# Optimization experiments

Measured on AMD Instinct MI355X. Metric: run time of the kernel, lower is better.

The kernel has to match this reference:

```python
import jax, jax.numpy as jnp
import numpy as np

RADIUS = 2.0      # ball radius (meters)
NSAMPLE = 32      # max neighbors per ball
B = 4             # number of scenes (batch)
NPB = 4096        # points per scene (equal counts assumed)
C = 20            # number of semantic classes
CUBE = 20.0       # points live in a [0,20]^3 m cube


def setup_inputs() -> dict:
    key = jax.random.key(0)
    k1, k2, k3 = jax.random.split(key, 3)
    xyz = jax.random.uniform(k1, (B * NPB, 3), jnp.float32) * CUBE
    pred = jax.random.normal(k2, (B * NPB, C), jnp.float32)
    labels = jax.random.randint(k3, (B * NPB,), 0, C)
    tgt = jax.nn.one_hot(labels, C, dtype=jnp.float32)
    cnt = jnp.full((B,), NPB, dtype=jnp.int32)
    # module asserts new_xyz == xyz and equal batch counts
    return {"xyz": xyz, "xyz_batch_cnt": cnt, "pred": pred, "tgt": tgt,
            "new_xyz": xyz, "new_xyz_batch_cnt": cnt}


def _ball_query(xyz_b, new_xyz_b, radius, nsample):
    """xyz_b, new_xyz_b: (B, n, 3). Returns local idx (B, n, nsample).
    Replicates pointnet2 stack ball_query: first `nsample` points (in index
    order) with squared distance < radius^2; unfilled slots repeat the first
    found index. Indices are local to each batch segment."""
    n = xyz_b.shape[1]
    d2 = jnp.sum((new_xyz_b[:, :, None, :] - xyz_b[:, None, :, :]) ** 2, axis=-1)  # (B,n,n)
    mask = d2 < radius * radius
    # score = point index if inside ball else sentinel n; smallest scores = first hits
    score = jnp.where(mask, jnp.arange(n, dtype=jnp.int32), jnp.int32(n))
    neg_vals, _ = jax.lax.top_k(-score, nsample)   # largest of -score == smallest score
    idx = -neg_vals                                # (B,n,nsample), ascending index order
    first = idx[:, :, :1]                          # first found index (self is always in-ball)
    idx = jnp.where(idx == n, first, idx)          # fill empty slots with first index
    return idx


def _group(feats_b, idx_b):
    """feats_b: (B, n, C); idx_b: (B, m, nsample) local indices -> (B, m, nsample, C)."""
    b = jnp.arange(feats_b.shape[0])[:, None, None]
    return feats_b[b, idx_b]


def reference(xyz, xyz_batch_cnt, pred, tgt, new_xyz, new_xyz_batch_cnt):
    nb = xyz_batch_cnt.shape[0]
    n = xyz.shape[0] // nb                 # equal per-batch counts
    xyz_b = xyz.reshape(nb, n, 3)
    new_xyz_b = new_xyz.reshape(nb, n, 3)

    idx_b = _ball_query(xyz_b, new_xyz_b, RADIUS, NSAMPLE)   # (B,n,ns)
    m = nb * n
    idx = idx_b.reshape(m, NSAMPLE)

    # grouping_operation -> (M, C, nsample)
    grouped_pred = _group(pred.reshape(nb, n, -1), idx_b).reshape(m, NSAMPLE, -1).transpose(0, 2, 1)
    grouped_tgt = _group(tgt.reshape(nb, n, -1), idx_b).reshape(m, NSAMPLE, -1).transpose(0, 2, 1)

    # since new_xyz == xyz, every ball contains its own center -> empty_ball_mask
    # is all-False and the nonempty filtering in the torch code is the identity.
    pred_local_relation = grouped_pred - pred[:, :, None]
    tgt_local_relation = grouped_tgt - tgt[:, :, None]

    # weight (computed under no_grad in torch)
    eq = idx == idx[:, :1]
    not_eq = ~eq
    not_eq = not_eq.at[:, 0].set(True)
    a = not_eq.astype(jnp.float32)
    weight = a / jnp.sum(a, axis=-1, keepdims=True)
    return (pred_local_relation, tgt_local_relation, weight)
```

## Files before the change

kernel.cpp:

```cpp
#include <hip/hip_runtime.h>

#define NS 32
#define GD 10
#define NCXY (GD * GD)
#define COLCAP 128
#define WCAP 64
#define INV_CELL 0.5f
#define MARGIN 1e-3f

static __device__ __forceinline__ int lane_rank(unsigned long long m) {
    return __builtin_amdgcn_mbcnt_hi((unsigned)(m >> 32),
                                     __builtin_amdgcn_mbcnt_lo((unsigned)m, 0u));
}

__global__ __launch_bounds__(256) void build_kernel(
    const float* __restrict__ xyz, int n,
    int* __restrict__ colOff, float4* __restrict__ pts)
{
    __shared__ float4 hl[4][WCAP];
    __shared__ int    swcnt[4];
    __shared__ float4 merged[COLCAP];

    const int col  = blockIdx.x;
    const int b    = col / NCXY;
    const int cxy  = col - b * NCXY;
    const int mycx = cxy / GD;
    const int mycy = cxy - mycx * GD;
    const int lane = threadIdx.x & 63;
    const int wv   = threadIdx.x >> 6;
    const float* __restrict__ px = xyz + (size_t)b * n * 3;

    const int per = (n + 3) >> 2;
    const int j0  = wv * per;
    const int j1  = min(j0 + per, n);
    int cnt = 0;
    for (int it = j0; it < j1; it += 64) {
        const int  j   = it + lane;
        const bool inb = j < j1;
        const int  jc  = inb ? j : 0;
        const float x = px[3 * jc], y = px[3 * jc + 1], z = px[3 * jc + 2];
        const int cx = min(max((int)floorf(x * INV_CELL), 0), GD - 1);
        const int cy = min(max((int)floorf(y * INV_CELL), 0), GD - 1);
        const bool hit = inb && (cx == mycx) && (cy == mycy);
        const unsigned long long m = __ballot(hit);
        if (m) {
            const int zc  = min(max((int)floorf(z * INV_CELL), 0), GD - 1);
            const int pos = cnt + lane_rank(m);
            if (hit && pos < WCAP)
                hl[wv][pos] = make_float4(x, y, z, __int_as_float((zc << 12) | j));
            cnt += __popcll(m);
        }
    }
    if (lane == 0) swcnt[wv] = cnt < WCAP ? cnt : WCAP;
    __syncthreads();

    const int p0 = swcnt[0], p1 = p0 + swcnt[1], p2 = p1 + swcnt[2], p3 = p2 + swcnt[3];
    const int h  = p3 < COLCAP ? p3 : COLCAP;
    if (wv == 0) {
        for (int g = lane; g < h; g += 64) {
            const int w   = (g >= p0) + (g >= p1) + (g >= p2);
            const int off = g - (w == 0 ? 0 : (w == 1 ? p0 : (w == 2 ? p1 : p2)));
            merged[g] = hl[w][off];
        }
    }
    __syncthreads();

    if (wv == 0) {
        int czc[GD];
        #pragma unroll
        for (int k = 0; k < GD; ++k) czc[k] = 0;
        for (int r = 0; r < h; r += 64) {
            const int t = r + lane;
            int zc = -1;
            if (t < h) zc = __float_as_int(merged[t].w) >> 12;
            #pragma unroll
            for (int k = 0; k < GD; ++k)
                czc[k] += __popcll(__ballot(zc == k));
        }
        int off[GD + 1];
        off[0] = 0;
        #pragma unroll
        for (int k = 0; k < GD; ++k) off[k + 1] = off[k] + czc[k];

        int cur[GD];
        #pragma unroll
        for (int k = 0; k < GD; ++k) cur[k] = off[k];

        for (int r = 0; r < h; r += 64) {
            const int t = r + lane;
            int zc = -1, pl = 0;
            float4 f = make_float4(0.f, 0.f, 0.f, 0.f);
            if (t < h) { f = merged[t]; pl = __float_as_int(f.w); zc = pl >> 12; }
            #pragma unroll
            for (int k = 0; k < GD; ++k) {
                const unsigned long long mk = __ballot(zc == k);
                if (zc == k) {
                    const int pos = cur[k] + lane_rank(mk);
                    pts[(size_t)col * COLCAP + pos] =
                        make_float4(f.x, f.y, f.z, __int_as_float(pl & 4095));
                }
                cur[k] += __popcll(mk);
            }
        }
        if (lane == 0) {
            const int bo = col * 11;
            #pragma unroll
            for (int k = 0; k < GD; ++k) colOff[bo + k] = off[k];
            colOff[bo + GD] = h;
        }
    }
}

template <int C>
__global__ __launch_bounds__(256) void query_kernel(
    const float* __restrict__ new_xyz,
    const float* __restrict__ pred, const float* __restrict__ tgt,
    const int* __restrict__ colOff, const float4* __restrict__ pts,
    int n, int total,
    float* __restrict__ out0, float* __restrict__ out1, float* __restrict__ wout)
{
#pragma clang fp contract(off)
    __shared__ int spref[4][17];
    __shared__ int sgb[4][16];
    __shared__ int slist[4][64];

    const int lane = threadIdx.x & 63;
    const int wv   = __builtin_amdgcn_readfirstlane(threadIdx.x >> 6);
    int q = blockIdx.x * 4 + wv;
    if (q >= total) q = total - 1;
    const int b    = q / n;
    const int base = b * n;

    const float qx = new_xyz[q * 3 + 0];
    const float qy = new_xyz[q * 3 + 1];
    const float qz = new_xyz[q * 3 + 2];

    int cx0 = max((int)floorf((qx - 2.0f - MARGIN) * INV_CELL), 0);
    int cx1 = min((int)floorf((qx + 2.0f + MARGIN) * INV_CELL), GD - 1);
    int cy0 = max((int)floorf((qy - 2.0f - MARGIN) * INV_CELL), 0);
    int cy1 = min((int)floorf((qy + 2.0f + MARGIN) * INV_CELL), GD - 1);
    int cz0 = max((int)floorf((qz - 2.0f - MARGIN) * INV_CELL), 0);
    int cz1 = min((int)floorf((qz + 2.0f + MARGIN) * INV_CELL), GD - 1);
    const int ny = cy1 - cy0 + 1;
    const int nrange = __builtin_amdgcn_readfirstlane((cx1 - cx0 + 1) * ny);

    int cc = 0, gb = 0;
    if (lane < nrange) {
        const int rx   = lane / ny;
        const int ry   = lane - rx * ny;
        const int ccol = b * NCXY + (cx0 + rx) * GD + (cy0 + ry);
        const int o0   = colOff[ccol * 11 + cz0];
        const int o1   = colOff[ccol * 11 + cz1 + 1];
        gb = ccol * COLCAP + o0;
        cc = o1 - o0;
    }
    int run = cc;
    #pragma unroll
    for (int off = 1; off < 64; off <<= 1) {
        int y = __shfl_up(run, off, 64);
        if (lane >= off) run += y;
    }
    const int T = __shfl(run, nrange - 1, 64);

    if (lane < 16) spref[wv][lane + 1] = run;
    if (lane == 0) spref[wv][0] = 0;
    if (lane < nrange) sgb[wv][lane] = gb;

    __syncthreads();

    int tot = 0;
    for (int r = 0; r < T; r += 64) {
        const int  t   = r + lane;
        const bool act = t < T;
        const int  tcl = act ? t : 0;
        int k = 0;
        #pragma unroll
        for (int step = 8; step >= 1; step >>= 1) {
            const int nk = k + step;
            if (spref[wv][nk] <= tcl) k = nk;
        }
        const int ai = sgb[wv][k] + (tcl - spref[wv][k]);
        const float4 f = pts[ai];
        float dx = qx - f.x, dy = qy - f.y, dz = qz - f.z;
        float d2 = (dx * dx + dy * dy) + dz * dz;
        const bool hit = act && (d2 < 4.0f);
        const unsigned long long m = __ballot(hit);
        const int pos = tot + lane_rank(m);
        if (hit && pos < 64) slist[wv][pos] = __float_as_int(f.w);
        tot += __popcll(m);
    }

    __syncthreads();

    const int totv = tot < 64 ? tot : 64;
    int v = (lane < totv) ? slist[wv][lane] : 0x7fffffff;
    const int l32 = lane & 31;
    if (totv <= 32) {
        #pragma unroll
        for (int k = 2; k <= 32; k <<= 1) {
            #pragma unroll
            for (int j = k >> 1; j >= 1; j >>= 1) {
                const int  o     = __shfl_xor(v, j, 32);
                const bool up    = ((l32 & k) == 0);
                const bool lower = ((l32 & j) == 0);
                const int  mn = v < o ? v : o;
                const int  mx = v < o ? o : v;
                v = (lower == up) ? mn : mx;
            }
        }
    } else {
        #pragma unroll
        for (int k = 2; k <= 64; k <<= 1) {
            #pragma unroll
            for (int j = k >> 1; j >= 1; j >>= 1) {
                const int  o     = __shfl_xor(v, j, 64);
                const bool up    = ((lane & k) == 0);
                const bool lower = ((lane & j) == 0);
                const int  mn = v < o ? v : o;
                const int  mx = v < o ? o : v;
                v = (lower == up) ? mn : mx;
            }
        }
    }

    const int tc     = tot < NS ? tot : NS;
    const int firstv = __shfl(v, 0, 64);
    const int first  = (tot > 0) ? firstv : (n - 1);
    const int s      = lane & 31;
    const int jl0    = __shfl(v, s, 64);
    const int jl     = (s < tc) ? jl0 : first;

    const int tcm = tc > 0 ? tc : 1;
    if (lane < NS)
        wout[(size_t)q * NS + lane] = (lane < tcm) ? 1.0f / (float)tcm : 0.0f;

    const float* __restrict__ src = (lane >> 5) ? tgt : pred;
    float* __restrict__ dst       = (lane >> 5) ? out1 : out0;
    const float4* __restrict__ nb = (const float4*)(src + (size_t)(base + jl) * C);
    const float4* __restrict__ ct = (const float4*)(src + (size_t)q * C);
    float* __restrict__ o = dst + (size_t)q * (C * NS) + s;
    #pragma unroll
    for (int c4 = 0; c4 < C / 4; ++c4) {
        const float4 a = nb[c4], bq = ct[c4];
        o[(c4 * 4 + 0) * NS] = a.x - bq.x;
        o[(c4 * 4 + 1) * NS] = a.y - bq.y;
        o[(c4 * 4 + 2) * NS] = a.z - bq.z;
        o[(c4 * 4 + 3) * NS] = a.w - bq.w;
    }
    #pragma unroll
    for (int c = (C / 4) * 4; c < C; ++c)
        o[c * NS] = src[(size_t)(base + jl) * C + c] - src[(size_t)q * C + c];
}

template <int C>
__global__ __launch_bounds__(256) void fused_brute_kernel(
    const float* __restrict__ xyz, const float* __restrict__ new_xyz,
    const float* __restrict__ pred, const float* __restrict__ tgt,
    int n, int total, float* __restrict__ out0, float* __restrict__ out1,
    float* __restrict__ wout)
{
#pragma clang fp contract(off)
    __shared__ int sidx[8][NS];

    const int lane = threadIdx.x & 63;
    const int wv   = __builtin_amdgcn_readfirstlane(threadIdx.x >> 6);
    int q0 = (blockIdx.x * 4 + wv) * 2;
    if (q0 > total - 2) q0 = total - 2;
    const int base = (q0 / n) * n;

    const float ax0 = new_xyz[q0 * 3 + 0], ay0 = new_xyz[q0 * 3 + 1], az0 = new_xyz[q0 * 3 + 2];
    const float ax1 = new_xyz[q0 * 3 + 3], ay1 = new_xyz[q0 * 3 + 4], az1 = new_xyz[q0 * 3 + 5];
    const float* __restrict__ px = xyz + (size_t)base * 3;

    int tot0 = 0, tot1 = 0, first0 = n - 1, first1 = n - 1;
    for (int it = 0; it < n; it += 64) {
        const int ja  = it + lane;
        const int jca = ja < n ? ja : n - 1;
        const float xa = px[jca * 3 + 0], ya = px[jca * 3 + 1], za = px[jca * 3 + 2];
        float dx = ax0 - xa, dy = ay0 - ya, dz = az0 - za;
        const float d0 = (dx * dx + dy * dy) + dz * dz;
        dx = ax1 - xa; dy = ay1 - ya; dz = az1 - za;
        const float d1 = (dx * dx + dy * dy) + dz * dz;
        const bool h0 = (ja < n) & (d0 < 4.0f);
        const bool h1 = (ja < n) & (d1 < 4.0f);
        const unsigned long long m0 = __ballot(h0);
        if (m0) {
            if (tot0 == 0) first0 = it + __builtin_ctzll(m0);
            const int pos = tot0 + lane_rank(m0);
            if (h0 && pos < NS) sidx[wv * 2 + 0][pos] = ja;
            tot0 += __popcll(m0);
        }
        const unsigned long long m1 = __ballot(h1);
        if (m1) {
            if (tot1 == 0) first1 = it + __builtin_ctzll(m1);
            const int pos = tot1 + lane_rank(m1);
            if (h1 && pos < NS) sidx[wv * 2 + 1][pos] = ja;
            tot1 += __popcll(m1);
        }
    }

    const int s  = lane & 31;
    const int qs = lane >> 5;
    {
        const int tt    = qs ? tot1 : tot0;
        const int first = qs ? first1 : first0;
        const int tc    = tt < NS ? tt : NS;
        if (s >= tc) sidx[wv * 2 + qs][s] = first;
        const int tcm = tc > 0 ? tc : 1;
        wout[(size_t)q0 * NS + lane] = (s < tcm) ? 1.0f / (float)tcm : 0.0f;
    }
    __syncthreads();

    const int q  = q0 + qs;
    const int jl = sidx[wv * 2 + qs][s];
    const float4* __restrict__ nb_p = (const float4*)(pred + (size_t)(base + jl) * C);
    const float4* __restrict__ nb_t = (const float4*)(tgt  + (size_t)(base + jl) * C);
    const float4* __restrict__ ct_p = (const float4*)(pred + (size_t)q * C);
    const float4* __restrict__ ct_t = (const float4*)(tgt  + (size_t)q * C);
    float* __restrict__ o0 = out0 + (size_t)q * (C * NS) + s;
    float* __restrict__ o1 = out1 + (size_t)q * (C * NS) + s;
    #pragma unroll
    for (int c4 = 0; c4 < C / 4; ++c4) {
        const float4 a = nb_p[c4], bq = ct_p[c4];
        o0[(c4 * 4 + 0) * NS] = a.x - bq.x;
        o0[(c4 * 4 + 1) * NS] = a.y - bq.y;
        o0[(c4 * 4 + 2) * NS] = a.z - bq.z;
        o0[(c4 * 4 + 3) * NS] = a.w - bq.w;
        const float4 u = nb_t[c4], vv = ct_t[c4];
        o1[(c4 * 4 + 0) * NS] = u.x - vv.x;
        o1[(c4 * 4 + 1) * NS] = u.y - vv.y;
        o1[(c4 * 4 + 2) * NS] = u.z - vv.z;
        o1[(c4 * 4 + 3) * NS] = u.w - vv.w;
    }
}

extern "C" void kernel_launch(void* const* d_in, const int* in_sizes, int n_in,
                              void* d_out, int out_size, void* d_ws, size_t ws_size,
                              hipStream_t stream)
{
    const float* xyz     = (const float*)d_in[0];
    const float* pred    = (const float*)d_in[2];
    const float* tgt     = (const float*)d_in[3];
    const float* new_xyz = (const float*)d_in[4];

    const int total = in_sizes[0] / 3;
    const int nb    = in_sizes[1];
    const int n     = total / nb;
    const int C     = in_sizes[2] / total;

    float* out = (float*)d_out;
    const size_t relsz = (size_t)total * C * NS;
    float* out0 = out;
    float* out1 = out + relsz;
    float* wout = out + 2 * relsz;

    const int ncols = nb * NCXY;
    const size_t ws_need = (size_t)ncols * COLCAP * sizeof(float4)
                         + (size_t)ncols * 11 * sizeof(int);

    if (C == 20 && ws_size >= ws_need) {
        float4* pts    = (float4*)d_ws;
        int*    colOff = (int*)((char*)d_ws + (size_t)ncols * COLCAP * sizeof(float4));

        build_kernel<<<ncols, 256, 0, stream>>>(xyz, n, colOff, pts);
        query_kernel<20><<<(total + 3) / 4, 256, 0, stream>>>(
            new_xyz, pred, tgt, colOff, pts, n, total, out0, out1, wout);
    } else if (C == 20) {
        fused_brute_kernel<20><<<(total + 7) / 8, 256, 0, stream>>>(
            xyz, new_xyz, pred, tgt, n, total, out0, out1, wout);
    }
    (void)n_in; (void)out_size;
}
```

Before: 37.17 us.

## Process two query points per wavefront in grid ball-query kernel

The query kernel now handles two queries per 64-lane wave. Cell ranges for both are scanned in half-waves, and candidate loads and distance tests for the two queries are interleaved in one loop. The neighbour lists are sorted with 32-lane bitonic sorts in parallel, then staged through shared memory so all 64 lanes write weights and gathered outputs for both queries. This aims to raise lane utilisation and memory-level parallelism, at the cost of more registers, an extra barrier, and a fallback to the brute-force kernel when n is not a multiple of 8.

```diff
diff --git a/kernel.cpp b/kernel.cpp
--- a/kernel.cpp
+++ b/kernel.cpp
@@ -112,7 +112,7 @@
 }
 
 template <int C>
-__global__ __launch_bounds__(256) void query_kernel(
+__global__ __launch_bounds__(256) void query2_kernel(
     const float* __restrict__ new_xyz,
     const float* __restrict__ pred, const float* __restrict__ tgt,
     const int* __restrict__ colOff, const float4* __restrict__ pts,
@@ -120,136 +120,188 @@
     float* __restrict__ out0, float* __restrict__ out1, float* __restrict__ wout)
 {
 #pragma clang fp contract(off)
-    __shared__ int spref[4][17];
-    __shared__ int sgb[4][16];
-    __shared__ int slist[4][64];
+    __shared__ int spref[4][2][17];
+    __shared__ int sgb[4][2][16];
+    __shared__ int slist[4][2][64];
+    __shared__ int sorted[4][2][32];
 
     const int lane = threadIdx.x & 63;
     const int wv   = __builtin_amdgcn_readfirstlane(threadIdx.x >> 6);
-    int q = blockIdx.x * 4 + wv;
-    if (q >= total) q = total - 1;
-    const int b    = q / n;
+    int q0w = blockIdx.x * 8 + wv * 2;
+    if (q0w > total - 2) q0w = total - 2;
+    const int b    = q0w / n;
     const int base = b * n;
 
-    const float qx = new_xyz[q * 3 + 0];
-    const float qy = new_xyz[q * 3 + 1];
-    const float qz = new_xyz[q * 3 + 2];
-
-    int cx0 = max((int)floorf((qx - 2.0f - MARGIN) * INV_CELL), 0);
-    int cx1 = min((int)floorf((qx + 2.0f + MARGIN) * INV_CELL), GD - 1);
-    int cy0 = max((int)floorf((qy - 2.0f - MARGIN) * INV_CELL), 0);
-    int cy1 = min((int)floorf((qy + 2.0f + MARGIN) * INV_CELL), GD - 1);
-    int cz0 = max((int)floorf((qz - 2.0f - MARGIN) * INV_CELL), 0);
-    int cz1 = min((int)floorf((qz + 2.0f + MARGIN) * INV_CELL), GD - 1);
-    const int ny = cy1 - cy0 + 1;
-    const int nrange = __builtin_amdgcn_readfirstlane((cx1 - cx0 + 1) * ny);
+    const float qx0 = new_xyz[q0w * 3 + 0], qy0 = new_xyz[q0w * 3 + 1], qz0 = new_xyz[q0w * 3 + 2];
+    const float qx1 = new_xyz[q0w * 3 + 3], qy1 = new_xyz[q0w * 3 + 4], qz1 = new_xyz[q0w * 3 + 5];
+
+    int cx0a = max((int)floorf((qx0 - 2.0f - MARGIN) * INV_CELL), 0);
+    int cx1a = min((int)floorf((qx0 + 2.0f + MARGIN) * INV_CELL), GD - 1);
+    int cy0a = max((int)floorf((qy0 - 2.0f - MARGIN) * INV_CELL), 0);
+    int cy1a = min((int)floorf((qy0 + 2.0f + MARGIN) * INV_CELL), GD - 1);
+    int cz0a = max((int)floorf((qz0 - 2.0f - MARGIN) * INV_CELL), 0);
+    int cz1a = min((int)floorf((qz0 + 2.0f + MARGIN) * INV_CELL), GD - 1);
+    const int nya = cy1a - cy0a + 1;
+    const int nr0 = __builtin_amdgcn_readfirstlane((cx1a - cx0a + 1) * nya);
+
+    int cx0b = max((int)floorf((qx1 - 2.0f - MARGIN) * INV_CELL), 0);
+    int cx1b = min((int)floorf((qx1 + 2.0f + MARGIN) * INV_CELL), GD - 1);
+    int cy0b = max((int)floorf((qy1 - 2.0f - MARGIN) * INV_CELL), 0);
+    int cy1b = min((int)floorf((qy1 + 2.0f + MARGIN) * INV_CELL), GD - 1);
+    int cz0b = max((int)floorf((qz1 - 2.0f - MARGIN) * INV_CELL), 0);
+    int cz1b = min((int)floorf((qz1 + 2.0f + MARGIN) * INV_CELL), GD - 1);
+    const int nyb = cy1b - cy0b + 1;
+    const int nr1 = __builtin_amdgcn_readfirstlane((cx1b - cx0b + 1) * nyb);
 
     int cc = 0, gb = 0;
-    if (lane < nrange) {
-        const int rx   = lane / ny;
-        const int ry   = lane - rx * ny;
-        const int ccol = b * NCXY + (cx0 + rx) * GD + (cy0 + ry);
-        const int o0   = colOff[ccol * 11 + cz0];
-        const int o1   = colOff[ccol * 11 + cz1 + 1];
+    if (lane < nr0) {
+        const int rx   = lane / nya;
+        const int ry   = lane - rx * nya;
+        const int ccol = b * NCXY + (cx0a + rx) * GD + (cy0a + ry);
+        const int o0   = colOff[ccol * 11 + cz0a];
+        const int o1   = colOff[ccol * 11 + cz1a + 1];
         gb = ccol * COLCAP + o0;
         cc = o1 - o0;
+    } else if (lane >= 32 && lane < 32 + nr1) {
+        const int r    = lane - 32;
+        const int rx   = r / nyb;
+        const int ry   = r - rx * nyb;
+        const int ccol = b * NCXY + (cx0b + rx) * GD + (cy0b + ry);
+        const int o0   = colOff[ccol * 11 + cz0b];
+        const int o1   = colOff[ccol * 11 + cz1b + 1];
+        gb = ccol * COLCAP + o0;
+        cc = o1 - o0;
     }
     int run = cc;
     #pragma unroll
-    for (int off = 1; off < 64; off <<= 1) {
+    for (int off = 1; off < 32; off <<= 1) {
         int y = __shfl_up(run, off, 64);
-        if (lane >= off) run += y;
-    }
-    const int T = __shfl(run, nrange - 1, 64);
-
-    if (lane < 16) spref[wv][lane + 1] = run;
-    if (lane == 0) spref[wv][0] = 0;
-    if (lane < nrange) sgb[wv][lane] = gb;
-
-    __syncthreads();
-
-    int tot = 0;
-    for (int r = 0; r < T; r += 64) {
-        const int  t   = r + lane;
-        const bool act = t < T;
-        const int  tcl = act ? t : 0;
-        int k = 0;
+        if ((lane & 31) >= off) run += y;
+    }
+    const int T0 = __shfl(run, nr0 - 1, 64);
+    const int T1 = __shfl(run, 32 + nr1 - 1, 64);
+
+    if (lane < 16) spref[wv][0][lane + 1] = run;
+    else if (lane >= 32 && lane < 48) spref[wv][1][lane - 31] = run;
+    if (lane == 0) { spref[wv][0][0] = 0; spref[wv][1][0] = 0; }
+    if (lane < nr0) sgb[wv][0][lane] = gb;
+    else if (lane >= 32 && lane < 32 + nr1) sgb[wv][1][lane - 32] = gb;
+
+    __syncthreads();
+
+    const int maxT = T0 > T1 ? T0 : T1;
+    int tot0 = 0, tot1 = 0;
+    for (int r = 0; r < maxT; r += 64) {
+        const int  t    = r + lane;
+        const bool actA = t < T0;
+        const bool actB = t < T1;
+        const int  tca  = actA ? t : 0;
+        const int  tcb  = actB ? t : 0;
+        int kA = 0, kB = 0;
         #pragma unroll
         for (int step = 8; step >= 1; step >>= 1) {
-            const int nk = k + step;
-            if (spref[wv][nk] <= tcl) k = nk;
-        }
-        const int ai = sgb[wv][k] + (tcl - spref[wv][k]);
-        const float4 f = pts[ai];
-        float dx = qx - f.x, dy = qy - f.y, dz = qz - f.z;
-        float d2 = (dx * dx + dy * dy) + dz * dz;
-        const bool hit = act && (d2 < 4.0f);
-        const unsigned long long m = __ballot(hit);
-        const int pos = tot + lane_rank(m);
-        if (hit && pos < 64) slist[wv][pos] = __float_as_int(f.w);
-        tot += __popcll(m);
-    }
-
-    __syncthreads();
-
-    const int totv = tot < 64 ? tot : 64;
-    int v = (lane < totv) ? slist[wv][lane] : 0x7fffffff;
-    const int l32 = lane & 31;
-    if (totv <= 32) {
+            if (spref[wv][0][kA + step] <= tca) kA += step;
+            if (spref[wv][1][kB + step] <= tcb) kB += step;
+        }
+        const int aiA = sgb[wv][0][kA] + (tca - spref[wv][0][kA]);
+        const int aiB = sgb[wv][1][kB] + (tcb - spref[wv][1][kB]);
+        const float4 fA = pts[aiA];
+        const float4 fB = pts[aiB];
+
+        float dxA = qx0 - fA.x, dyA = qy0 - fA.y, dzA = qz0 - fA.z;
+        const float d2A = (dxA * dxA + dyA * dyA) + dzA * dzA;
+        float dxB = qx1 - fB.x, dyB = qy1 - fB.y, dzB = qz1 - fB.z;
+        const float d2B = (dxB * dxB + dyB * dyB) + dzB * dzB;
+        const bool hitA = actA && (d2A < 4.0f);
+        const bool hitB = actB && (d2B < 4.0f);
+
+        const unsigned long long mA = __ballot(hitA);
+        const int posA = tot0 + lane_rank(mA);
+        if (hitA && posA < 64) slist[wv][0][posA] = __float_as_int(fA.w);
+        tot0 += __popcll(mA);
+        const unsigned long long mB = __ballot(hitB);
+        const int posB = tot1 + lane_rank(mB);
+        if (hitB && posB < 64) slist[wv][1][posB] = __float_as_int(fB.w);
+        tot1 += __popcll(mB);
+    }
+
+    __syncthreads();
+
+    const int qs = lane >> 5;
+    const int s  = lane & 31;
+    if (tot0 <= 32 && tot1 <= 32) {
+        const int totq = qs ? tot1 : tot0;
+        int v = (s < totq) ? slist[wv][qs][s] : 0x7fffffff;
         #pragma unroll
         for (int k = 2; k <= 32; k <<= 1) {
             #pragma unroll
             for (int j = k >> 1; j >= 1; j >>= 1) {
                 const int  o     = __shfl_xor(v, j, 32);
-                const bool up    = ((l32 & k) == 0);
-                const bool lower = ((l32 & j) == 0);
+                const bool up    = ((s & k) == 0);
+                const bool lower = ((s & j) == 0);
                 const int  mn = v < o ? v : o;
                 const int  mx = v < o ? o : v;
                 v = (lower == up) ? mn : mx;
             }
         }
+        sorted[wv][qs][s] = v;
     } else {
-        #pragma unroll
-        for (int k = 2; k <= 64; k <<= 1) {
+        #pragma unroll 1
+        for (int qq = 0; qq < 2; ++qq) {
+            const int totq = qq ? tot1 : tot0;
+            const int totv = totq < 64 ? totq : 64;
+            int v = (lane < totv) ? slist[wv][qq][lane] : 0x7fffffff;
             #pragma unroll
-            for (int j = k >> 1; j >= 1; j >>= 1) {
-                const int  o     = __shfl_xor(v, j, 64);
-                const bool up    = ((lane & k) == 0);
-                const bool lower = ((lane & j) == 0);
-                const int  mn = v < o ? v : o;
-                const int  mx = v < o ? o : v;
-                v = (lower == up) ? mn : mx;
+            for (int k = 2; k <= 64; k <<= 1) {
+                #pragma unroll
+                for (int j = k >> 1; j >= 1; j >>= 1) {
+                    const int  o     = __shfl_xor(v, j, 64);
+                    const bool up    = ((lane & k) == 0);
+                    const bool lower = ((lane & j) == 0);
+                    const int  mn = v < o ? v : o;
+                    const int  mx = v < o ? o : v;
+                    v = (lower == up) ? mn : mx;
+                }
             }
-        }
-    }
-
-    const int tc     = tot < NS ? tot : NS;
-    const int firstv = __shfl(v, 0, 64);
-    const int first  = (tot > 0) ? firstv : (n - 1);
-    const int s      = lane & 31;
-    const int jl0    = __shfl(v, s, 64);
-    const int jl     = (s < tc) ? jl0 : first;
-
-    const int tcm = tc > 0 ? tc : 1;
-    if (lane < NS)
-        wout[(size_t)q * NS + lane] = (lane < tcm) ? 1.0f / (float)tcm : 0.0f;
-
-    const float* __restrict__ src = (lane >> 5) ? tgt : pred;
-    float* __restrict__ dst       = (lane >> 5) ? out1 : out0;
-    const float4* __restrict__ nb = (const float4*)(src + (size_t)(base + jl) * C);
-    const float4* __restrict__ ct = (const float4*)(src + (size_t)q * C);
-    float* __restrict__ o = dst + (size_t)q * (C * NS) + s;
+            if (lane < 32) sorted[wv][qq][lane] = v;
+        }
+    }
+
+    __syncthreads();
+
+    const int tc0 = tot0 < NS ? tot0 : NS;
+    const int tc1 = tot1 < NS ? tot1 : NS;
+    {
+        const int tcq = qs ? tc1 : tc0;
+        const int tcm = tcq > 0 ? tcq : 1;
+        wout[(size_t)q0w * NS + lane] = (s < tcm) ? 1.0f / (float)tcm : 0.0f;
+    }
+
+    const float* __restrict__ src = qs ? tgt : pred;
+    float* __restrict__ dst       = qs ? out1 : out0;
     #pragma unroll
-    for (int c4 = 0; c4 < C / 4; ++c4) {
-        const float4 a = nb[c4], bq = ct[c4];
-        o[(c4 * 4 + 0) * NS] = a.x - bq.x;
-        o[(c4 * 4 + 1) * NS] = a.y - bq.y;
-        o[(c4 * 4 + 2) * NS] = a.z - bq.z;
-        o[(c4 * 4 + 3) * NS] = a.w - bq.w;
-    }
-    #pragma unroll
-    for (int c = (C / 4) * 4; c < C; ++c)
-        o[c * NS] = src[(size_t)(base + jl) * C + c] - src[(size_t)q * C + c];
+    for (int qq = 0; qq < 2; ++qq) {
+        const int qg    = q0w + qq;
+        const int totq  = qq ? tot1 : tot0;
+        const int tcq   = qq ? tc1 : tc0;
+        const int first = (totq > 0) ? sorted[wv][qq][0] : (n - 1);
+        const int jl    = (s < tcq) ? sorted[wv][qq][s] : first;
+
+        const float4* __restrict__ nb = (const float4*)(src + (size_t)(base + jl) * C);
+        const float4* __restrict__ ct = (const float4*)(src + (size_t)qg * C);
+        float* __restrict__ o = dst + (size_t)qg * (C * NS) + s;
+        #pragma unroll
+        for (int c4 = 0; c4 < C / 4; ++c4) {
+            const float4 a = nb[c4], bq = ct[c4];
+            o[(c4 * 4 + 0) * NS] = a.x - bq.x;
+            o[(c4 * 4 + 1) * NS] = a.y - bq.y;
+            o[(c4 * 4 + 2) * NS] = a.z - bq.z;
+            o[(c4 * 4 + 3) * NS] = a.w - bq.w;
+        }
+        #pragma unroll
+        for (int c = (C / 4) * 4; c < C; ++c)
+            o[c * NS] = src[(size_t)(base + jl) * C + c] - src[(size_t)qg * C + c];
+    }
 }
 
 template <int C>
@@ -358,12 +410,12 @@
     const size_t ws_need = (size_t)ncols * COLCAP * sizeof(float4)
                          + (size_t)ncols * 11 * sizeof(int);
 
-    if (C == 20 && ws_size >= ws_need) {
+    if (C == 20 && (n % 8) == 0 && ws_size >= ws_need) {
         float4* pts    = (float4*)d_ws;
         int*    colOff = (int*)((char*)d_ws + (size_t)ncols * COLCAP * sizeof(float4));
 
         build_kernel<<<ncols, 256, 0, stream>>>(xyz, n, colOff, pts);
-        query_kernel<20><<<(total + 3) / 4, 256, 0, stream>>>(
+        query2_kernel<20><<<(total + 7) / 8, 256, 0, stream>>>(
             new_xyz, pred, tgt, colOff, pts, n, total, out0, out1, wout);
     } else if (C == 20) {
         fused_brute_kernel<20><<<(total + 7) / 8, 256, 0, stream>>>(
```

Measured after the change: 36.39 us. -2.1%, faster.
